# Kernel tuning notes

Hardware: AMD Instinct MI355X
Metric: run time of the kernel (lower is better)

The kernel has to match this reference:

```python
import jax, jax.numpy as jnp
import numpy as np

INPUT_DIM = 256
HIDDEN_DIM = 512
BATCH = 64
SEQ = 512


def setup_inputs() -> dict:
    key = jax.random.key(0)
    k1, k2, k3, k4, k5 = jax.random.split(key, 5)
    s = 1.0 / np.sqrt(HIDDEN_DIM)
    x = jax.random.normal(k1, (BATCH, SEQ, INPUT_DIM), dtype=jnp.float32)
    # PyTorch GRU param layout: [3*H, in] with gate order (r, z, n)
    W_ih = jax.random.uniform(k2, (3 * HIDDEN_DIM, INPUT_DIM), minval=-s, maxval=s, dtype=jnp.float32)
    W_hh = jax.random.uniform(k3, (3 * HIDDEN_DIM, HIDDEN_DIM), minval=-s, maxval=s, dtype=jnp.float32)
    b_ih = jax.random.uniform(k4, (3 * HIDDEN_DIM,), minval=-s, maxval=s, dtype=jnp.float32)
    b_hh = jax.random.uniform(k5, (3 * HIDDEN_DIM,), minval=-s, maxval=s, dtype=jnp.float32)
    return {"x": x, "W_ih": W_ih, "W_hh": W_hh, "b_ih": b_ih, "b_hh": b_hh}


def _gru_last(x, W_ih, W_hh, b_ih, b_hh):
    B, T, _ = x.shape
    H = W_hh.shape[1]
    # Precompute input projections for all timesteps: [B, T, 3H]
    x_proj = jnp.einsum('bti,gi->btg', x, W_ih) + b_ih
    x_proj = jnp.swapaxes(x_proj, 0, 1)  # [T, B, 3H] for scan

    def step(h, xp):
        h_proj = h @ W_hh.T + b_hh  # [B, 3H]
        xr, xz, xn = jnp.split(xp, 3, axis=-1)
        hr, hz, hn = jnp.split(h_proj, 3, axis=-1)
        r = jax.nn.sigmoid(xr + hr)
        z = jax.nn.sigmoid(xz + hz)
        n = jnp.tanh(xn + r * hn)
        h_new = (1.0 - z) * n + z * h
        return h_new, None

    h0 = jnp.zeros((B, H), dtype=x.dtype)
    h_last, _ = jax.lax.scan(step, h0, x_proj)
    return h_last  # equals output[:, -1, :] for unidirectional single-layer GRU


def reference(x, W_ih, W_hh, b_ih, b_hh):
    return _gru_last(x, W_ih, W_hh, b_ih, b_hh)
```

## Files before the change

### kernel.cpp

```cpp
#include <hip/hip_runtime.h>
#include <hip/hip_bf16.h>


#define NB 64
#define NT 512
#define NI 256
#define NH 512

typedef __attribute__((ext_vector_type(8))) short bf16x8;
typedef __attribute__((ext_vector_type(4))) float f32x4;
typedef __attribute__((ext_vector_type(4))) int i32x4;

static __device__ __forceinline__ short f2b(float f) {
  unsigned u = __builtin_bit_cast(unsigned, f);
  unsigned r = (u + 0x7fffu + ((u >> 16) & 1u)) >> 16;
  return (short)r;
}
static __device__ __forceinline__ float sigm(float x) {
  return 1.0f / (1.0f + __expf(-x));
}
static __device__ __forceinline__ float tanh_f(float x) {
  return 1.0f - 2.0f / (__expf(2.0f * x) + 1.0f);
}

#define ISSUE16(R)                                                            \
  do {                                                                        \
    _Pragma("unroll") for (int i_ = 0; i_ < 16; i_++) {                       \
      const int kk2 = (i_ + (R)) & 15;                                        \
      const void* ap_ =                                                       \
          (const char*)hcur + (size_t)(((kk2 * 4 + q) * 64 + b0) << 4);       \
      asm volatile("global_load_dwordx4 %0, %1, off sc1"                      \
                   : "=v"(hv[kk2]) : "v"(ap_));                               \
    }                                                                         \
  } while (0)

__global__ __launch_bounds__(256, 1)
void gru_persistent(const float* __restrict__ x,
                    const float* __restrict__ Wih,
                    const float* __restrict__ Whh,
                    const float* __restrict__ bih,
                    const float* __restrict__ bhh,
                    float* __restrict__ out,
                    unsigned char* __restrict__ ws) {
  const int wg   = blockIdx.x;
  const int tid  = threadIdx.x;
  const int wave = tid >> 6;
  const int lane = tid & 63;
  const int c    = lane & 15;
  const int q    = lane >> 4;

  const unsigned long long t0 = __builtin_amdgcn_s_memrealtime();

  unsigned long long* flags = (unsigned long long*)ws;
  int* tags = (int*)(ws + 8192);
  unsigned short* hb0 = (unsigned short*)(ws + 16384);
  unsigned short* hb1 = (unsigned short*)(ws + 16384 + 65536);
  unsigned short* xb  = (unsigned short*)(ws + 16384 + 2 * 65536);

  __shared__ __align__(16) unsigned short trans[4][16][8];

  {
    const float4* x4 = (const float4*)x;
    const int total4 = NB * NT * NI / 4;
    const int nthr = NB * 256;
    for (int i = wg * 256 + tid; i < total4; i += nthr) {
      float4 v = x4[i];
      ushort4 o;
      o.x = (unsigned short)f2b(v.x);
      o.y = (unsigned short)f2b(v.y);
      o.z = (unsigned short)f2b(v.z);
      o.w = (unsigned short)f2b(v.w);
      ((ushort4*)xb)[i] = o;
    }
    ((unsigned int*)hb0)[wg * 256 + tid] = 0u;
    if (wg == 0) {
#pragma unroll
      for (int r2 = 0; r2 < 4; r2++) tags[r2 * 256 + tid] = 0;
    }
  }

  bf16x8 wh[2][16];
  bf16x8 wi[2][8];
#pragma unroll
  for (int nt = 0; nt < 2; nt++) {
    int nl = nt * 16 + c;
    bool valid = nl < 24;
    int gate = nl >> 3;
    int jj = nl & 7;
    int grow = valid ? (gate * NH + wg * 8 + jj) : 0;
#pragma unroll
    for (int kk = 0; kk < 16; kk++) {
      const float* p = Whh + (size_t)grow * NH + kk * 32 + q * 8;
      bf16x8 f;
#pragma unroll
      for (int e = 0; e < 8; e++) f[e] = valid ? f2b(p[e]) : (short)0;
      wh[nt][kk] = f;
    }
#pragma unroll
    for (int kk = 0; kk < 8; kk++) {
      const float* p = Wih + (size_t)grow * NI + kk * 32 + q * 8;
      bf16x8 f;
#pragma unroll
      for (int e = 0; e < 8; e++) f[e] = valid ? f2b(p[e]) : (short)0;
      wi[nt][kk] = f;
    }
  }

  const int jcol = wg * 8 + (c & 7);
  const float bri = bih[jcol],          brh = bhh[jcol];
  const float bzi = bih[NH + jcol],     bzh = bhh[NH + jcol];
  const float bni = bih[2 * NH + jcol], bnh = bhh[2 * NH + jcol];

  float hold[4] = {0.f, 0.f, 0.f, 0.f};

  __syncthreads();
  if (tid == 0)
    __hip_atomic_store(&flags[wg * 8], __builtin_amdgcn_s_memrealtime(),
                       __ATOMIC_RELEASE, __HIP_MEMORY_SCOPE_AGENT);
  if (wave == 0) {
    while (__hip_atomic_load(&flags[lane * 8], __ATOMIC_RELAXED,
                             __HIP_MEMORY_SCOPE_AGENT) < t0)
      __builtin_amdgcn_s_sleep(1);
  }
  __syncthreads();
  __threadfence();

  const int b0 = wave * 16 + c;
  const int rot = wg & 7;
  const int* tagp = tags + (wg & 3) * 256 + wave * 64 + lane;

  for (int t = 0; t < NT; t++) {
    const unsigned short* hcur = (t & 1) ? hb1 : hb0;
    unsigned short* hnext      = (t & 1) ? hb0 : hb1;

    f32x4 aX0 = {0.f, 0.f, 0.f, 0.f}, aX1 = {0.f, 0.f, 0.f, 0.f};
    f32x4 aH0 = {0.f, 0.f, 0.f, 0.f}, aH1 = {0.f, 0.f, 0.f, 0.f};

    const bf16x8* xr = (const bf16x8*)(xb + ((size_t)b0 * NT + t) * NI);

#pragma unroll
    for (int kk = 0; kk < 8; kk++) {
      bf16x8 a = xr[kk * 4 + q];
      aX0 = __builtin_amdgcn_mfma_f32_16x16x32_bf16(a, wi[0][kk], aX0, 0, 0, 0);
      aX1 = __builtin_amdgcn_mfma_f32_16x16x32_bf16(a, wi[1][kk], aX1, 0, 0, 0);
    }

    if (t > 0) {
      const int need = t + 1;
      for (;;) {
        int v;
        asm volatile("global_load_dword %0, %1, off sc1"
                     : "=v"(v) : "v"(tagp));
        asm volatile("s_waitcnt vmcnt(0)" : "+v"(v)::"memory");
        if (__all(v >= need)) break;
      }
    }

    i32x4 hv[16];
    if      (rot == 0) ISSUE16(0);
    else if (rot == 1) ISSUE16(2);
    else if (rot == 2) ISSUE16(4);
    else if (rot == 3) ISSUE16(6);
    else if (rot == 4) ISSUE16(8);
    else if (rot == 5) ISSUE16(10);
    else if (rot == 6) ISSUE16(12);
    else               ISSUE16(14);
    asm volatile("s_waitcnt vmcnt(0)"
                 : "+v"(hv[0]), "+v"(hv[1]), "+v"(hv[2]), "+v"(hv[3]),
                   "+v"(hv[4]), "+v"(hv[5]), "+v"(hv[6]), "+v"(hv[7]),
                   "+v"(hv[8]), "+v"(hv[9]), "+v"(hv[10]), "+v"(hv[11]),
                   "+v"(hv[12]), "+v"(hv[13]), "+v"(hv[14]), "+v"(hv[15])
                 ::"memory");

#pragma unroll
    for (int kk = 0; kk < 16; kk++) {
      bf16x8 a = __builtin_bit_cast(bf16x8, hv[kk]);
      aH0 = __builtin_amdgcn_mfma_f32_16x16x32_bf16(a, wh[0][kk], aH0, 0, 0, 0);
      aH1 = __builtin_amdgcn_mfma_f32_16x16x32_bf16(a, wh[1][kk], aH1, 0, 0, 0);
    }

#pragma unroll
    for (int r = 0; r < 4; r++) {
      float xz = __shfl_xor(aX0[r], 8, 64);
      float hz = __shfl_xor(aH0[r], 8, 64);
      float rr = sigm(aX0[r] + bri + aH0[r] + brh);
      float zz = sigm(xz + bzi + hz + bzh);
      float nn = tanh_f(aX1[r] + bni + rr * (aH1[r] + bnh));
      float hv2 = (1.0f - zz) * nn + zz * hold[r];
      hold[r] = hv2;
      if (c < 8) trans[wave][q * 4 + r][c] = (unsigned short)f2b(hv2);
    }

    if (t < NT - 1) {
      asm volatile("s_waitcnt lgkmcnt(0)" ::: "memory");
      if (lane < 16) {
        int b = wave * 16 + lane;
        i32x4 pk = *(const i32x4*)&trans[wave][lane][0];
        void* dst = (char*)hnext + ((size_t)(wg * 64 + b) << 4);
        asm volatile("global_store_dwordx4 %0, %1, off sc1"
                     :: "v"(dst), "v"(pk) : "memory");
      }
      asm volatile("s_waitcnt vmcnt(0)" ::: "memory");
      if (lane == 0) {
#pragma unroll
        for (int r2 = 0; r2 < 4; r2++)
          __hip_atomic_store(&tags[r2 * 256 + wave * 64 + wg], t + 2,
                             __ATOMIC_RELAXED, __HIP_MEMORY_SCOPE_AGENT);
      }
    }
  }

  if (c < 8) {
#pragma unroll
    for (int r = 0; r < 4; r++) {
      int b = wave * 16 + q * 4 + r;
      out[(size_t)b * NH + wg * 8 + c] = hold[r];
    }
  }
}

extern "C" void kernel_launch(void* const* d_in, const int* in_sizes, int n_in,
                              void* d_out, int out_size, void* d_ws, size_t ws_size,
                              hipStream_t stream) {
  const float* x   = (const float*)d_in[0];
  const float* Wih = (const float*)d_in[1];
  const float* Whh = (const float*)d_in[2];
  const float* bih = (const float*)d_in[3];
  const float* bhh = (const float*)d_in[4];
  float* out = (float*)d_out;
  hipLaunchKernelGGL(gru_persistent, dim3(NB), dim3(256), 0, stream,
                     x, Wih, Whh, bih, bhh, out, (unsigned char*)d_ws);
}
```

Baseline: 1.917 ms.

## Split GRU workgroups by batch group and stage shared hidden state in LDS

Each workgroup now owns 16 batch rows and 32 hidden columns (one 8-column slice per wave), instead of all 64 batches for 8 columns. Synchronisation is therefore confined to the 16 workgroups of a batch group. The previous-step hidden state for those 16 batches is loaded once per workgroup with coalesced 16-byte loads into an LDS buffer, rather than each wave separately gathering 16 KB from global memory. This cuts the per-step global hidden-state traffic and the number of tags each workgroup must poll, but adds an LDS round trip and a block-wide barrier on every timestep.

```diff
diff --git a/kernel.cpp b/kernel.cpp
--- a/kernel.cpp
+++ b/kernel.cpp
@@ -22,17 +22,6 @@
 static __device__ __forceinline__ float tanh_f(float x) {
   return 1.0f - 2.0f / (__expf(2.0f * x) + 1.0f);
 }
-
-#define ISSUE16(R)                                                            \
-  do {                                                                        \
-    _Pragma("unroll") for (int i_ = 0; i_ < 16; i_++) {                       \
-      const int kk2 = (i_ + (R)) & 15;                                        \
-      const void* ap_ =                                                       \
-          (const char*)hcur + (size_t)(((kk2 * 4 + q) * 64 + b0) << 4);       \
-      asm volatile("global_load_dwordx4 %0, %1, off sc1"                      \
-                   : "=v"(hv[kk2]) : "v"(ap_));                               \
-    }                                                                         \
-  } while (0)
 
 __global__ __launch_bounds__(256, 1)
 void gru_persistent(const float* __restrict__ x,
@@ -48,6 +37,8 @@
   const int lane = tid & 63;
   const int c    = lane & 15;
   const int q    = lane >> 4;
+  const int g    = wg & 3;
+  const int cp   = wg >> 2;
 
   const unsigned long long t0 = __builtin_amdgcn_s_memrealtime();
 
@@ -57,6 +48,7 @@
   unsigned short* hb1 = (unsigned short*)(ws + 16384 + 65536);
   unsigned short* xb  = (unsigned short*)(ws + 16384 + 2 * 65536);
 
+  __shared__ __align__(16) unsigned short hstage[16][520];
   __shared__ __align__(16) unsigned short trans[4][16][8];
 
   {
@@ -73,10 +65,7 @@
       ((ushort4*)xb)[i] = o;
     }
     ((unsigned int*)hb0)[wg * 256 + tid] = 0u;
-    if (wg == 0) {
-#pragma unroll
-      for (int r2 = 0; r2 < 4; r2++) tags[r2 * 256 + tid] = 0;
-    }
+    if (wg == 0) tags[tid] = 0;
   }
 
   bf16x8 wh[2][16];
@@ -87,7 +76,7 @@
     bool valid = nl < 24;
     int gate = nl >> 3;
     int jj = nl & 7;
-    int grow = valid ? (gate * NH + wg * 8 + jj) : 0;
+    int grow = valid ? (gate * NH + cp * 32 + wave * 8 + jj) : 0;
 #pragma unroll
     for (int kk = 0; kk < 16; kk++) {
       const float* p = Whh + (size_t)grow * NH + kk * 32 + q * 8;
@@ -106,7 +95,7 @@
     }
   }
 
-  const int jcol = wg * 8 + (c & 7);
+  const int jcol = cp * 32 + wave * 8 + (c & 7);
   const float bri = bih[jcol],          brh = bhh[jcol];
   const float bzi = bih[NH + jcol],     bzh = bhh[NH + jcol];
   const float bni = bih[2 * NH + jcol], bnh = bhh[2 * NH + jcol];
@@ -125,9 +114,8 @@
   __syncthreads();
   __threadfence();
 
-  const int b0 = wave * 16 + c;
-  const int rot = wg & 7;
-  const int* tagp = tags + (wg & 3) * 256 + wave * 64 + lane;
+  const int b0 = g * 16 + c;
+  const int* tagp = tags + g * 64 + lane;
 
   for (int t = 0; t < NT; t++) {
     const unsigned short* hcur = (t & 1) ? hb1 : hb0;
@@ -156,25 +144,29 @@
       }
     }
 
-    i32x4 hv[16];
-    if      (rot == 0) ISSUE16(0);
-    else if (rot == 1) ISSUE16(2);
-    else if (rot == 2) ISSUE16(4);
-    else if (rot == 3) ISSUE16(6);
-    else if (rot == 4) ISSUE16(8);
-    else if (rot == 5) ISSUE16(10);
-    else if (rot == 6) ISSUE16(12);
-    else               ISSUE16(14);
-    asm volatile("s_waitcnt vmcnt(0)"
-                 : "+v"(hv[0]), "+v"(hv[1]), "+v"(hv[2]), "+v"(hv[3]),
-                   "+v"(hv[4]), "+v"(hv[5]), "+v"(hv[6]), "+v"(hv[7]),
-                   "+v"(hv[8]), "+v"(hv[9]), "+v"(hv[10]), "+v"(hv[11]),
-                   "+v"(hv[12]), "+v"(hv[13]), "+v"(hv[14]), "+v"(hv[15])
-                 ::"memory");
+    {
+      i32x4 hl0, hl1, hl2, hl3;
+      const char* src = (const char*)hcur + (size_t)g * 16384;
+      const void* a0 = src + ((size_t)(0 * 256 + tid) << 4);
+      const void* a1 = src + ((size_t)(1 * 256 + tid) << 4);
+      const void* a2 = src + ((size_t)(2 * 256 + tid) << 4);
+      const void* a3 = src + ((size_t)(3 * 256 + tid) << 4);
+      asm volatile("global_load_dwordx4 %0, %1, off sc1" : "=v"(hl0) : "v"(a0));
+      asm volatile("global_load_dwordx4 %0, %1, off sc1" : "=v"(hl1) : "v"(a1));
+      asm volatile("global_load_dwordx4 %0, %1, off sc1" : "=v"(hl2) : "v"(a2));
+      asm volatile("global_load_dwordx4 %0, %1, off sc1" : "=v"(hl3) : "v"(a3));
+      asm volatile("s_waitcnt vmcnt(0)"
+                   : "+v"(hl0), "+v"(hl1), "+v"(hl2), "+v"(hl3) :: "memory");
+      *(i32x4*)&hstage[(0 * 256 + tid) >> 6][((0 * 256 + tid) & 63) * 8] = hl0;
+      *(i32x4*)&hstage[(1 * 256 + tid) >> 6][((1 * 256 + tid) & 63) * 8] = hl1;
+      *(i32x4*)&hstage[(2 * 256 + tid) >> 6][((2 * 256 + tid) & 63) * 8] = hl2;
+      *(i32x4*)&hstage[(3 * 256 + tid) >> 6][((3 * 256 + tid) & 63) * 8] = hl3;
+    }
+    __syncthreads();
 
 #pragma unroll
     for (int kk = 0; kk < 16; kk++) {
-      bf16x8 a = __builtin_bit_cast(bf16x8, hv[kk]);
+      bf16x8 a = *(const bf16x8*)&hstage[c][kk * 32 + q * 8];
       aH0 = __builtin_amdgcn_mfma_f32_16x16x32_bf16(a, wh[0][kk], aH0, 0, 0, 0);
       aH1 = __builtin_amdgcn_mfma_f32_16x16x32_bf16(a, wh[1][kk], aH1, 0, 0, 0);
     }
@@ -194,27 +186,24 @@
     if (t < NT - 1) {
       asm volatile("s_waitcnt lgkmcnt(0)" ::: "memory");
       if (lane < 16) {
-        int b = wave * 16 + lane;
         i32x4 pk = *(const i32x4*)&trans[wave][lane][0];
-        void* dst = (char*)hnext + ((size_t)(wg * 64 + b) << 4);
+        void* dst = (char*)hnext + (size_t)(g * 16 + lane) * 1024 +
+                    (size_t)cp * 64 + (size_t)wave * 16;
         asm volatile("global_store_dwordx4 %0, %1, off sc1"
                      :: "v"(dst), "v"(pk) : "memory");
       }
       asm volatile("s_waitcnt vmcnt(0)" ::: "memory");
-      if (lane == 0) {
-#pragma unroll
-        for (int r2 = 0; r2 < 4; r2++)
-          __hip_atomic_store(&tags[r2 * 256 + wave * 64 + wg], t + 2,
-                             __ATOMIC_RELAXED, __HIP_MEMORY_SCOPE_AGENT);
-      }
+      if (lane == 0)
+        __hip_atomic_store(&tags[g * 64 + cp * 4 + wave], t + 2,
+                           __ATOMIC_RELAXED, __HIP_MEMORY_SCOPE_AGENT);
     }
   }
 
   if (c < 8) {
 #pragma unroll
     for (int r = 0; r < 4; r++) {
-      int b = wave * 16 + q * 4 + r;
-      out[(size_t)b * NH + wg * 8 + c] = hold[r];
+      int b = g * 16 + q * 4 + r;
+      out[(size_t)b * NH + cp * 32 + wave * 8 + c] = hold[r];
     }
   }
 }
```

Measured after the change: 1.937 ms. No clear change (+1.0%).
